# Kernel tuning notes

Hardware: AMD Instinct MI355X
Metric: run time of the kernel (lower is better)

Reference implementation:

```python
import jax, jax.numpy as jnp
import numpy as np

N_NODES = 100000
N_EDGES = 3200000
D = 128
BN_EPS = 1e-5


def setup_inputs() -> dict:
    key = jax.random.key(0)
    k1, k2, k3, k4 = jax.random.split(key, 4)
    x = jax.random.normal(k1, (N_NODES, D), dtype=jnp.float32)
    edge_index = jax.random.randint(k2, (2, N_EDGES), 0, N_NODES, dtype=jnp.int64)
    # GCNConv linear weight, torch nn.Linear convention: [out_dim, in_dim]
    W = jax.random.normal(k3, (D, D), dtype=jnp.float32) * (1.0 / np.sqrt(D))
    # BatchNorm1d affine params
    gamma = jnp.ones((D,), dtype=jnp.float32) + 0.1 * jax.random.normal(k4, (D,), dtype=jnp.float32)
    beta = jnp.zeros((D,), dtype=jnp.float32)
    return {"x": x, "edge_index": edge_index, "W": W, "gamma": gamma, "beta": beta}


def reference(x, edge_index, W, gamma, beta):
    # GCNConv(bias=False, add_self_loops=False), then BN (batch stats), ReLU, skip-add.
    src, dst = edge_index[0], edge_index[1]
    n = x.shape[0]

    # linear transform: [N, D_out]
    h = x @ W.T

    # symmetric GCN normalization: deg over destination, norm = d^-1/2[src]*d^-1/2[dst]
    ones = jnp.ones((src.shape[0],), dtype=x.dtype)
    deg = jax.ops.segment_sum(ones, dst, num_segments=n)
    dinv = jnp.where(deg > 0, jax.lax.rsqrt(jnp.maximum(deg, 1.0)), 0.0)
    norm = dinv[src] * dinv[dst]  # [E]

    # gather-message-scatter: [E, D] -> [N, D]
    msg = h[src] * norm[:, None]
    agg = jax.ops.segment_sum(msg, dst, num_segments=n)

    # BatchNorm1d in training mode (batch statistics, biased variance)
    mean = jnp.mean(agg, axis=0)
    var = jnp.mean(jnp.square(agg - mean), axis=0)
    bn = (agg - mean) * jax.lax.rsqrt(var + BN_EPS) * gamma + beta

    # ReLU + residual skip (dims match)
    out = jax.nn.relu(bn) + x
    return out
```

## Files before the change

### kernel.cpp

```cpp
#include <hip/hip_runtime.h>
#include <hip/hip_bf16.h>
#include <cstdint>
#include <cstddef>

#define D 128
#define SBBITS 10
#define NSB 128
#define TILE 4096
#define BINT 512
#define NSLOT 64
#define AGGB 2048

typedef __attribute__((ext_vector_type(8))) short short8;
typedef __attribute__((ext_vector_type(4))) float f32x4;

__device__ __forceinline__ unsigned short f2bf(float f) {
    union { float f; unsigned u; } v; v.f = f;
    unsigned r = v.u + 0x7FFF + ((v.u >> 16) & 1);
    return (unsigned short)(r >> 16);
}
__device__ __forceinline__ float bflo(unsigned p) {
    union { unsigned u; float f; } v; v.u = p << 16; return v.f;
}
__device__ __forceinline__ float bfhi(unsigned p) {
    union { unsigned u; float f; } v; v.u = p & 0xFFFF0000u; return v.f;
}

__global__ __launch_bounds__(256) void k_prep(const unsigned* __restrict__ ei, int E,
                                              int* __restrict__ flag,
                                              const float* __restrict__ W,
                                              unsigned short* __restrict__ Wbf,
                                              int* __restrict__ g_sbcnt,
                                              float* __restrict__ part2) {
    int t = threadIdx.x, b = blockIdx.x;
    int i = b * 256 + t;
    if (i < D * D) Wbf[i] = f2bf(W[i]);
    part2[i] = 0.f;
    if (b == 0 && t == 0) {
        int n = E < 256 ? E : 256;
        int allz = 1;
        for (int k = 0; k < n; ++k) {
            if (ei[2 * k + 1] != 0u) { allz = 0; break; }
        }
        *flag = allz;
    }
    if (b == 63 && t < NSB) g_sbcnt[t] = 0;
}

__global__ __launch_bounds__(256) void k_gemm(const float* __restrict__ x,
                                              const unsigned short* __restrict__ Wbf,
                                              unsigned short* __restrict__ h, int M) {
    __shared__ unsigned short sx[64 * 136];
    int t = threadIdx.x;
    int base = blockIdx.x * 64;

#pragma unroll
    for (int j = 0; j < 8; ++j) {
        int idx = j * 256 + t;
        int row = idx >> 5, c4 = (idx & 31) * 4;
        int gr = base + row;
        float4 v = (gr < M) ? *(const float4*)(x + (size_t)gr * D + c4)
                            : make_float4(0.f, 0.f, 0.f, 0.f);
        unsigned short* dst = &sx[row * 136 + c4];
        dst[0] = f2bf(v.x); dst[1] = f2bf(v.y); dst[2] = f2bf(v.z); dst[3] = f2bf(v.w);
    }
    __syncthreads();

    int wave = t >> 6, lane = t & 63;
    int lr = lane & 15, lg = lane >> 4;
    int lrow = wave * 16 + lr;
    f32x4 acc[8];
#pragma unroll
    for (int i = 0; i < 8; ++i) acc[i] = (f32x4){0.f, 0.f, 0.f, 0.f};

#pragma unroll
    for (int ks = 0; ks < 4; ++ks) {
        int k0 = ks * 32 + lg * 8;
        short8 af = *(const short8*)(&sx[lrow * 136 + k0]);
#pragma unroll
        for (int nt = 0; nt < 8; ++nt) {
            short8 bf = *(const short8*)(Wbf + (size_t)(nt * 16 + lr) * D + k0);
            acc[nt] = __builtin_amdgcn_mfma_f32_16x16x32_bf16(af, bf, acc[nt], 0, 0, 0);
        }
    }
    int m0 = base + wave * 16;
#pragma unroll
    for (int nt = 0; nt < 8; ++nt) {
#pragma unroll
        for (int r = 0; r < 4; ++r) {
            int rr = m0 + lg * 4 + r;
            if (rr < M) h[(size_t)rr * D + nt * 16 + lr] = f2bf(acc[nt][r]);
        }
    }
}

__global__ __launch_bounds__(BINT) void k_bin(const int* __restrict__ ei, int E,
                                              const int* __restrict__ flagp,
                                              int* __restrict__ g_sbcnt,
                                              unsigned* __restrict__ binned, int C2) {
    __shared__ unsigned stage[TILE];
    __shared__ unsigned char ssb[TILE];
    __shared__ int hcnt[NSB], hoff[NSB], lcur[NSB], gbase[NSB];
    int f64 = *flagp;
    int t = threadIdx.x;
    int base = blockIdx.x * TILE;
    int cnt = E - base; if (cnt > TILE) cnt = TILE;

    if (t < NSB) hcnt[t] = 0;
    __syncthreads();

    unsigned ent[8]; int esb[8];
#pragma unroll
    for (int j = 0; j < 8; ++j) {
        int idx = j * BINT + t;
        esb[j] = -1;
        if (idx < cnt) {
            int e = base + idx;
            int s, d;
            if (f64) {
                s = ((const int2*)ei)[e].x;
                d = ((const int2*)ei)[E + e].x;
            } else {
                s = ei[e];
                d = ei[E + e];
            }
            esb[j] = d >> SBBITS;
            ent[j] = (unsigned)s | ((unsigned)(d & ((1 << SBBITS) - 1)) << 17);
            atomicAdd(&hcnt[esb[j]], 1);
        }
    }
    __syncthreads();
    if (t < NSB) hoff[t] = hcnt[t];
    __syncthreads();
#pragma unroll
    for (int off = 1; off < NSB; off <<= 1) {
        int a = (t < NSB && t >= off) ? hoff[t - off] : 0;
        __syncthreads();
        if (t < NSB) hoff[t] += a;
        __syncthreads();
    }
    if (t < NSB) {
        int ex = hoff[t] - hcnt[t];
        lcur[t] = ex;
        hoff[t] = ex;
        gbase[t] = (hcnt[t] > 0) ? atomicAdd(&g_sbcnt[t], hcnt[t]) : 0;
    }
    __syncthreads();
#pragma unroll
    for (int j = 0; j < 8; ++j) {
        if (esb[j] >= 0) {
            int p = atomicAdd(&lcur[esb[j]], 1);
            stage[p] = ent[j];
            ssb[p] = (unsigned char)esb[j];
        }
    }
    __syncthreads();
    for (int i = t; i < cnt; i += BINT) {
        int sb = ssb[i];
        int pos = gbase[sb] + (i - hoff[sb]);
        if (pos < C2) binned[(size_t)sb * C2 + pos] = stage[i];
    }
}

__global__ __launch_bounds__(1024) void k_fill2(const unsigned* __restrict__ binned, int C2,
                                                const int* __restrict__ g_sbcnt,
                                                int2* __restrict__ ronode,
                                                float* __restrict__ dinv,
                                                int* __restrict__ csrc, int N) {
    __shared__ int deg[1024];
    __shared__ int scn[1024];
    __shared__ int cur[1024];
    int b = blockIdx.x, t = threadIdx.x;
    int cnt = g_sbcnt[b]; if (cnt > C2) cnt = C2;
    const unsigned* ent = binned + (size_t)b * C2;

    deg[t] = 0;
    __syncthreads();
    for (int i = t; i < cnt; i += 1024) atomicAdd(&deg[ent[i] >> 17], 1);
    __syncthreads();
    scn[t] = deg[t];
    __syncthreads();
    for (int off = 1; off < 1024; off <<= 1) {
        int a = (t >= off) ? scn[t - off] : 0;
        __syncthreads();
        scn[t] += a;
        __syncthreads();
    }
    int ex = scn[t] - deg[t];
    cur[t] = ex;
    int node = (b << SBBITS) + t;
    if (node < N) {
        ronode[node] = make_int2(b * C2 + ex, deg[t]);
        dinv[node] = deg[t] > 0 ? rsqrtf((float)deg[t]) : 0.0f;
    }
    __syncthreads();
    for (int i = t; i < cnt; i += 1024) {
        unsigned e = ent[i];
        int pos = atomicAdd(&cur[e >> 17], 1);
        csrc[b * C2 + pos] = (int)(e & 0x1FFFF);
    }
}

__global__ __launch_bounds__(256) void k_agg(const unsigned long long* __restrict__ h,
                                             const int* __restrict__ csrc,
                                             const int2* __restrict__ ronode,
                                             const float* __restrict__ dinv,
                                             float4* __restrict__ out,
                                             float* __restrict__ part2, int N) {
    __shared__ float ssum[128], ssq[128];
    int t = threadIdx.x;
    int wave = t >> 6, lane = t & 63;
    int half = lane >> 5, lq = lane & 31;
    if (t < 128) { ssum[t] = 0.f; ssq[t] = 0.f; }

    float ps0 = 0.f, ps1 = 0.f, ps2 = 0.f, ps3 = 0.f;
    float pq0 = 0.f, pq1 = 0.f, pq2 = 0.f, pq3 = 0.f;

    for (int node = blockIdx.x * 4 + wave; node < N; node += AGGB * 4) {
        int2 ro = ronode[node];
        int beg = ro.x, end = ro.x + ro.y;
        float a0 = 0.f, a1 = 0.f, a2 = 0.f, a3 = 0.f;
        int i = beg;
        for (; i + 16 <= end; i += 16) {
#pragma unroll
            for (int p = 0; p < 8; ++p) {
                int e = i + 2 * p + half;
                int s = csrc[e];
                float w = dinv[s];
                unsigned long long pk = h[(size_t)s * 32 + lq];
                unsigned lo = (unsigned)pk, hi = (unsigned)(pk >> 32);
                a0 += w * bflo(lo); a1 += w * bfhi(lo);
                a2 += w * bflo(hi); a3 += w * bfhi(hi);
            }
        }
        for (; i + 2 <= end; i += 2) {
            int e = i + half;
            int s = csrc[e];
            float w = dinv[s];
            unsigned long long pk = h[(size_t)s * 32 + lq];
            unsigned lo = (unsigned)pk, hi = (unsigned)(pk >> 32);
            a0 += w * bflo(lo); a1 += w * bfhi(lo);
            a2 += w * bflo(hi); a3 += w * bfhi(hi);
        }
        if (i < end) {
            int s = csrc[i];
            float w = half ? 0.f : dinv[s];
            unsigned long long pk = h[(size_t)s * 32 + lq];
            unsigned lo = (unsigned)pk, hi = (unsigned)(pk >> 32);
            a0 += w * bflo(lo); a1 += w * bfhi(lo);
            a2 += w * bflo(hi); a3 += w * bfhi(hi);
        }
        a0 += __shfl_xor(a0, 32);
        a1 += __shfl_xor(a1, 32);
        a2 += __shfl_xor(a2, 32);
        a3 += __shfl_xor(a3, 32);
        float sd = dinv[node];
        float v0 = a0 * sd, v1 = a1 * sd, v2 = a2 * sd, v3 = a3 * sd;
        if (half == 0) {
            out[(size_t)node * 32 + lq] = make_float4(v0, v1, v2, v3);
            ps0 += v0; ps1 += v1; ps2 += v2; ps3 += v3;
            pq0 += v0 * v0; pq1 += v1 * v1; pq2 += v2 * v2; pq3 += v3 * v3;
        }
    }
    __syncthreads();
    if (half == 0) {
        int c = lq * 4;
        atomicAdd(&ssum[c],     ps0); atomicAdd(&ssq[c],     pq0);
        atomicAdd(&ssum[c + 1], ps1); atomicAdd(&ssq[c + 1], pq1);
        atomicAdd(&ssum[c + 2], ps2); atomicAdd(&ssq[c + 2], pq2);
        atomicAdd(&ssum[c + 3], ps3); atomicAdd(&ssq[c + 3], pq3);
    }
    __syncthreads();
    int slot = blockIdx.x & (NSLOT - 1);
    if (t < 128)       atomicAdd(&part2[slot * 256 + t], ssum[t]);
    else if (t < 256)  atomicAdd(&part2[slot * 256 + t], ssq[t - 128]);
}

__global__ void k_params(const float* __restrict__ part2, const float* __restrict__ gamma,
                         const float* __restrict__ beta, float* __restrict__ params, int N) {
    int t = threadIdx.x;
    float a = 0.f;
    for (int s = 0; s < NSLOT; ++s) a += part2[s * 256 + t];
    __shared__ float sh[256];
    sh[t] = a;
    __syncthreads();
    if (t < 128) {
        float mean = sh[t] / (float)N;
        float var = sh[128 + t] / (float)N - mean * mean;
        var = var > 0.f ? var : 0.f;
        float sc = gamma[t] * rsqrtf(var + 1e-5f);
        params[t] = sc;
        params[128 + t] = beta[t] - mean * sc;
    }
}

__global__ __launch_bounds__(256) void k_final(float4* __restrict__ out,
                                               const float4* __restrict__ x,
                                               const float* __restrict__ params, int n4) {
    const float4* p4 = (const float4*)params;
    for (int i = blockIdx.x * 256 + threadIdx.x; i < n4; i += gridDim.x * 256) {
        int c = i & 31;
        float4 s = p4[c], b = p4[32 + c];
        float4 v = out[i], xv = x[i];
        float4 r;
        r.x = fmaxf(v.x * s.x + b.x, 0.f) + xv.x;
        r.y = fmaxf(v.y * s.y + b.y, 0.f) + xv.y;
        r.z = fmaxf(v.z * s.z + b.z, 0.f) + xv.z;
        r.w = fmaxf(v.w * s.w + b.w, 0.f) + xv.w;
        out[i] = r;
    }
}

extern "C" void kernel_launch(void* const* d_in, const int* in_sizes, int n_in,
                              void* d_out, int out_size, void* d_ws, size_t ws_size,
                              hipStream_t stream) {
    const float* x     = (const float*)d_in[0];
    const int*   ei    = (const int*)d_in[1];
    const float* W     = (const float*)d_in[2];
    const float* gamma = (const float*)d_in[3];
    const float* beta  = (const float*)d_in[4];

    int N = in_sizes[0] / D;
    int E = in_sizes[1] / 2;
    int NSBu = (N + (1 << SBBITS) - 1) >> SBBITS;
    int avg = (E + NSBu - 1) / NSBu;
    int C2 = ((avg + 4096 + 63) / 64) * 64;

    char* ws = (char*)d_ws;
    size_t off = 0;
    auto alloc = [&](size_t bytes) { size_t o = off; off = (off + bytes + 255) & ~(size_t)255; return o; };

    unsigned short* h    = (unsigned short*)(ws + alloc((size_t)N * D * 2));
    int*      csrc   = (int*)     (ws + alloc((size_t)NSBu * C2 * 4));
    unsigned* binned = (unsigned*)(ws + alloc((size_t)NSBu * C2 * 4));
    int*      g_sbcnt= (int*)     (ws + alloc((size_t)NSB * 4));
    float*    dinv   = (float*)   (ws + alloc((size_t)N * 4));
    int2*     ronode = (int2*)    (ws + alloc((size_t)N * 8));
    float*    part2  = (float*)   (ws + alloc((size_t)NSLOT * 256 * 4));
    float*    params = (float*)   (ws + alloc(256 * 4));
    int*      flagp  = (int*)     (ws + alloc(4));
    unsigned short* Wbf = (unsigned short*)(ws + alloc((size_t)D * D * 2));

    k_prep<<<64, 256, 0, stream>>>((const unsigned*)ei, E, flagp, W, Wbf, g_sbcnt, part2);
    k_gemm<<<(N + 63) / 64, 256, 0, stream>>>(x, Wbf, h, N);
    k_bin<<<(E + TILE - 1) / TILE, BINT, 0, stream>>>(ei, E, flagp, g_sbcnt, binned, C2);
    k_fill2<<<NSBu, 1024, 0, stream>>>(binned, C2, g_sbcnt, ronode, dinv, csrc, N);
    k_agg<<<AGGB, 256, 0, stream>>>((const unsigned long long*)h, csrc, ronode, dinv,
                                    (float4*)d_out, part2, N);
    k_params<<<1, 256, 0, stream>>>(part2, gamma, beta, params, N);
    k_final<<<2048, 256, 0, stream>>>((float4*)d_out, (const float4*)x, params,
                                      (N * D) / 4);
}
```

Measured before the change: 396.7 us.

## Split BN statistics out of aggregation into separate stats kernel, one wave per node

The aggregation kernel now launches one wave per node instead of a persistent grid-stride loop. It drops the fused per-block BN sum and sum-of-squares accumulation and its shared and global atomics, and adds a 32-edge unrolled inner loop. A new k_stats kernel re-reads the 51MB aggregate to compute per-column partial sums, which k_params reduces over 512 blocks. This removes atomics and register pressure from the gather kernel but adds a full extra read of the output.

After: 401.6 us. Within noise of the previous version (+1.2%).

```diff
diff --git a/kernel.cpp b/kernel.cpp
--- a/kernel.cpp
+++ b/kernel.cpp
@@ -4,12 +4,11 @@
 #include <cstddef>
 
 #define D 128
+#define SBLK 512
 #define SBBITS 10
 #define NSB 128
 #define TILE 4096
 #define BINT 512
-#define NSLOT 64
-#define AGGB 2048
 
 typedef __attribute__((ext_vector_type(8))) short short8;
 typedef __attribute__((ext_vector_type(4))) float f32x4;
@@ -30,12 +29,10 @@
                                               int* __restrict__ flag,
                                               const float* __restrict__ W,
                                               unsigned short* __restrict__ Wbf,
-                                              int* __restrict__ g_sbcnt,
-                                              float* __restrict__ part2) {
+                                              int* __restrict__ g_sbcnt) {
     int t = threadIdx.x, b = blockIdx.x;
     int i = b * 256 + t;
     if (i < D * D) Wbf[i] = f2bf(W[i]);
-    part2[i] = 0.f;
     if (b == 0 && t == 0) {
         int n = E < 256 ? E : 256;
         int allz = 1;
@@ -205,36 +202,19 @@
                                              const int* __restrict__ csrc,
                                              const int2* __restrict__ ronode,
                                              const float* __restrict__ dinv,
-                                             float4* __restrict__ out,
-                                             float* __restrict__ part2, int N) {
-    __shared__ float ssum[128], ssq[128];
-    int t = threadIdx.x;
-    int wave = t >> 6, lane = t & 63;
+                                             float4* __restrict__ out, int N) {
+    int wave = threadIdx.x >> 6, lane = threadIdx.x & 63;
+    int node = blockIdx.x * 4 + wave;
+    if (node >= N) return;
     int half = lane >> 5, lq = lane & 31;
-    if (t < 128) { ssum[t] = 0.f; ssq[t] = 0.f; }
-
-    float ps0 = 0.f, ps1 = 0.f, ps2 = 0.f, ps3 = 0.f;
-    float pq0 = 0.f, pq1 = 0.f, pq2 = 0.f, pq3 = 0.f;
-
-    for (int node = blockIdx.x * 4 + wave; node < N; node += AGGB * 4) {
-        int2 ro = ronode[node];
-        int beg = ro.x, end = ro.x + ro.y;
-        float a0 = 0.f, a1 = 0.f, a2 = 0.f, a3 = 0.f;
-        int i = beg;
-        for (; i + 16 <= end; i += 16) {
-#pragma unroll
-            for (int p = 0; p < 8; ++p) {
-                int e = i + 2 * p + half;
-                int s = csrc[e];
-                float w = dinv[s];
-                unsigned long long pk = h[(size_t)s * 32 + lq];
-                unsigned lo = (unsigned)pk, hi = (unsigned)(pk >> 32);
-                a0 += w * bflo(lo); a1 += w * bfhi(lo);
-                a2 += w * bflo(hi); a3 += w * bfhi(hi);
-            }
-        }
-        for (; i + 2 <= end; i += 2) {
-            int e = i + half;
+    int2 ro = ronode[node];
+    int beg = ro.x, end = ro.x + ro.y;
+    float a0 = 0.f, a1 = 0.f, a2 = 0.f, a3 = 0.f;
+    int i = beg;
+    for (; i + 32 <= end; i += 32) {
+#pragma unroll
+        for (int p = 0; p < 16; ++p) {
+            int e = i + 2 * p + half;
             int s = csrc[e];
             float w = dinv[s];
             unsigned long long pk = h[(size_t)s * 32 + lq];
@@ -242,45 +222,69 @@
             a0 += w * bflo(lo); a1 += w * bfhi(lo);
             a2 += w * bflo(hi); a3 += w * bfhi(hi);
         }
-        if (i < end) {
-            int s = csrc[i];
-            float w = half ? 0.f : dinv[s];
+    }
+    if (i + 16 <= end) {
+#pragma unroll
+        for (int p = 0; p < 8; ++p) {
+            int e = i + 2 * p + half;
+            int s = csrc[e];
+            float w = dinv[s];
             unsigned long long pk = h[(size_t)s * 32 + lq];
             unsigned lo = (unsigned)pk, hi = (unsigned)(pk >> 32);
             a0 += w * bflo(lo); a1 += w * bfhi(lo);
             a2 += w * bflo(hi); a3 += w * bfhi(hi);
         }
-        a0 += __shfl_xor(a0, 32);
-        a1 += __shfl_xor(a1, 32);
-        a2 += __shfl_xor(a2, 32);
-        a3 += __shfl_xor(a3, 32);
-        float sd = dinv[node];
-        float v0 = a0 * sd, v1 = a1 * sd, v2 = a2 * sd, v3 = a3 * sd;
-        if (half == 0) {
-            out[(size_t)node * 32 + lq] = make_float4(v0, v1, v2, v3);
-            ps0 += v0; ps1 += v1; ps2 += v2; ps3 += v3;
-            pq0 += v0 * v0; pq1 += v1 * v1; pq2 += v2 * v2; pq3 += v3 * v3;
-        }
-    }
-    __syncthreads();
-    if (half == 0) {
-        int c = lq * 4;
-        atomicAdd(&ssum[c],     ps0); atomicAdd(&ssq[c],     pq0);
-        atomicAdd(&ssum[c + 1], ps1); atomicAdd(&ssq[c + 1], pq1);
-        atomicAdd(&ssum[c + 2], ps2); atomicAdd(&ssq[c + 2], pq2);
-        atomicAdd(&ssum[c + 3], ps3); atomicAdd(&ssq[c + 3], pq3);
-    }
-    __syncthreads();
-    int slot = blockIdx.x & (NSLOT - 1);
-    if (t < 128)       atomicAdd(&part2[slot * 256 + t], ssum[t]);
-    else if (t < 256)  atomicAdd(&part2[slot * 256 + t], ssq[t - 128]);
-}
-
-__global__ void k_params(const float* __restrict__ part2, const float* __restrict__ gamma,
+        i += 16;
+    }
+    for (; i + 2 <= end; i += 2) {
+        int e = i + half;
+        int s = csrc[e];
+        float w = dinv[s];
+        unsigned long long pk = h[(size_t)s * 32 + lq];
+        unsigned lo = (unsigned)pk, hi = (unsigned)(pk >> 32);
+        a0 += w * bflo(lo); a1 += w * bfhi(lo);
+        a2 += w * bflo(hi); a3 += w * bfhi(hi);
+    }
+    if (i < end) {
+        int s = csrc[i];
+        float w = half ? 0.f : dinv[s];
+        unsigned long long pk = h[(size_t)s * 32 + lq];
+        unsigned lo = (unsigned)pk, hi = (unsigned)(pk >> 32);
+        a0 += w * bflo(lo); a1 += w * bfhi(lo);
+        a2 += w * bflo(hi); a3 += w * bfhi(hi);
+    }
+    a0 += __shfl_xor(a0, 32);
+    a1 += __shfl_xor(a1, 32);
+    a2 += __shfl_xor(a2, 32);
+    a3 += __shfl_xor(a3, 32);
+    float sd = dinv[node];
+    if (half == 0)
+        out[(size_t)node * 32 + lq] = make_float4(a0 * sd, a1 * sd, a2 * sd, a3 * sd);
+}
+
+__global__ __launch_bounds__(256) void k_stats(const float* __restrict__ agg,
+                                               float* __restrict__ part, int N) {
+    int t = threadIdx.x;
+    int c = t & 127, half = t >> 7;
+    float s = 0.f, q = 0.f;
+    for (int r = blockIdx.x * 2 + half; r < N; r += SBLK * 2) {
+        float v = agg[(size_t)r * 128 + c];
+        s += v; q += v * v;
+    }
+    __shared__ float sh[512];
+    sh[t] = s; sh[256 + t] = q;
+    __syncthreads();
+    if (t < 128) {
+        part[blockIdx.x * 256 + t]       = sh[t] + sh[t + 128];
+        part[blockIdx.x * 256 + 128 + t] = sh[256 + t] + sh[256 + t + 128];
+    }
+}
+
+__global__ void k_params(const float* __restrict__ part, const float* __restrict__ gamma,
                          const float* __restrict__ beta, float* __restrict__ params, int N) {
     int t = threadIdx.x;
     float a = 0.f;
-    for (int s = 0; s < NSLOT; ++s) a += part2[s * 256 + t];
+    for (int b = 0; b < SBLK; ++b) a += part[b * 256 + t];
     __shared__ float sh[256];
     sh[t] = a;
     __syncthreads();
@@ -336,18 +340,21 @@
     int*      g_sbcnt= (int*)     (ws + alloc((size_t)NSB * 4));
     float*    dinv   = (float*)   (ws + alloc((size_t)N * 4));
     int2*     ronode = (int2*)    (ws + alloc((size_t)N * 8));
-    float*    part2  = (float*)   (ws + alloc((size_t)NSLOT * 256 * 4));
+    float*    part   = (float*)   (ws + alloc((size_t)SBLK * 256 * 4));
     float*    params = (float*)   (ws + alloc(256 * 4));
     int*      flagp  = (int*)     (ws + alloc(4));
     unsigned short* Wbf = (unsigned short*)(ws + alloc((size_t)D * D * 2));
 
-    k_prep<<<64, 256, 0, stream>>>((const unsigned*)ei, E, flagp, W, Wbf, g_sbcnt, part2);
+    float* outf = (float*)d_out;
+
+    k_prep<<<64, 256, 0, stream>>>((const unsigned*)ei, E, flagp, W, Wbf, g_sbcnt);
     k_gemm<<<(N + 63) / 64, 256, 0, stream>>>(x, Wbf, h, N);
     k_bin<<<(E + TILE - 1) / TILE, BINT, 0, stream>>>(ei, E, flagp, g_sbcnt, binned, C2);
     k_fill2<<<NSBu, 1024, 0, stream>>>(binned, C2, g_sbcnt, ronode, dinv, csrc, N);
-    k_agg<<<AGGB, 256, 0, stream>>>((const unsigned long long*)h, csrc, ronode, dinv,
-                                    (float4*)d_out, part2, N);
-    k_params<<<1, 256, 0, stream>>>(part2, gamma, beta, params, N);
+    k_agg<<<(N + 3) / 4, 256, 0, stream>>>((const unsigned long long*)h, csrc, ronode, dinv,
+                                           (float4*)d_out, N);
+    k_stats<<<SBLK, 256, 0, stream>>>(outf, part, N);
+    k_params<<<1, 256, 0, stream>>>(part, gamma, beta, params, N);
     k_final<<<2048, 256, 0, stream>>>((float4*)d_out, (const float4*)x, params,
                                       (N * D) / 4);
 }
```
